# Kernel tuning notes

Measured on AMD Instinct MI355X. Metric: run time of the kernel, lower is better.

The kernel has to match this reference:

```python
import jax, jax.numpy as jnp
import numpy as np

SCALE = 0.08838834764831845  # 1/sqrt(output_dim=128)


def setup_inputs() -> dict:
    key = jax.random.key(0)
    ks = jax.random.split(key, 7)
    N, D, H, E = 4096, 1024, 8, 128
    s = 0.02
    return {
        "X": jax.random.normal(ks[0], (N, D), jnp.float32),
        "Wq": jax.random.normal(ks[1], (H, D, E), jnp.float32) * s,
        "bq": jax.random.normal(ks[2], (H, E), jnp.float32) * s,
        "Wk": jax.random.normal(ks[3], (H, D, E), jnp.float32) * s,
        "bk": jax.random.normal(ks[4], (H, E), jnp.float32) * s,
        "Wv": jax.random.normal(ks[5], (H, D, E), jnp.float32) * s,
        "bv": jax.random.normal(ks[6], (H, E), jnp.float32) * s,
    }


def reference(X, Wq, bq, Wk, bk, Wv, bv):
    # per-head projections, batched over heads: [H, N, E]
    q = jnp.einsum("nd,hde->hne", X, Wq) + bq[:, None, :]
    k = jnp.einsum("nd,hde->hne", X, Wk) + bk[:, None, :]
    v = jnp.einsum("nd,hde->hne", X, Wv) + bv[:, None, :]
    # score[h, n, m] = scale * q[h,n,:] . k[h,m,:]  ([H, N, N])
    score = SCALE * jnp.einsum("hne,hme->hnm", q, k)
    # NOTE: original uses nn.Softmax(dim=0) on the [N, N] per-head matrix,
    # i.e. normalization over the QUERY (row) axis -> axis=1 here.
    attn = jax.nn.softmax(score, axis=1)
    # z[h, n, e] = sum_m attn[h,n,m] * v[h,m,e]
    z = jnp.einsum("hnm,hme->hne", attn, v)
    # concat heads along feature dim: [N, H*E]
    H, N, E = z.shape
    Z = jnp.transpose(z, (1, 0, 2)).reshape(N, H * E)
    return jax.nn.sigmoid(Z)
```

## Files before the change

kernel.cpp:

```cpp
#include <hip/hip_runtime.h>
#include <hip/hip_bf16.h>
#include <stdint.h>

typedef __bf16 bf16_t;
typedef __bf16 bf16x4 __attribute__((ext_vector_type(4)));
typedef __bf16 bf16x8 __attribute__((ext_vector_type(8)));
typedef float f32x4 __attribute__((ext_vector_type(4)));

#define MFMA_16x16x32(A, B, C) __builtin_amdgcn_mfma_f32_16x16x32_bf16(A, B, C, 0, 0, 0)
#define EXP2(x) __builtin_amdgcn_exp2f(x)

static constexpr float kScale = 0.08838834764831845f;
static constexpr float kLog2e = 1.4426950408889634f;
static constexpr float kC1 = kScale * kLog2e;

__device__ __forceinline__ void lds_cp16(void* lds, const void* g) {
  __builtin_amdgcn_global_load_lds(
      (__attribute__((address_space(1))) void*)(uintptr_t)g,
      (__attribute__((address_space(3))) void*)(uintptr_t)lds, 16, 0, 0);
}

template <int R, int K>
__device__ __forceinline__ void stage_tile(bf16_t* lds, const bf16_t* g, int ldg, int tid) {
  constexpr int TOT = R * K;
  constexpr int CH = R * 32;
  constexpr int ITERS = TOT / 2048;
  const int wave = tid >> 6;
#pragma unroll
  for (int i = 0; i < ITERS; ++i) {
    int linear = i * 2048 + tid * 8;
    int chunk = linear / CH;
    int rem = linear % CH;
    int r = rem >> 5;
    int c = rem & 31;
    lds_cp16(lds + i * 2048 + wave * 512, g + r * ldg + chunk * 32 + c);
  }
}

__device__ __forceinline__ bf16x8 frag_ld(const bf16_t* lds_chunk, int row, int lane) {
  return *(const bf16x8*)(lds_chunk + row * 32 + ((lane >> 4) << 3));
}

__device__ __forceinline__ bf16x8 p_transpose(f32x4 pa, f32x4 pb, bool hi16) {
  uint32_t a0, a1, b0, b1;
  asm("v_cvt_pk_bf16_f32 %0, %1, %2" : "=v"(a0) : "v"(pa[0]), "v"(pa[1]));
  asm("v_cvt_pk_bf16_f32 %0, %1, %2" : "=v"(a1) : "v"(pa[2]), "v"(pa[3]));
  asm("v_cvt_pk_bf16_f32 %0, %1, %2" : "=v"(b0) : "v"(pb[0]), "v"(pb[1]));
  asm("v_cvt_pk_bf16_f32 %0, %1, %2" : "=v"(b1) : "v"(pb[2]), "v"(pb[3]));
  asm("v_permlane32_swap_b32 %0, %1" : "+v"(a0), "+v"(b0));
  asm("v_permlane32_swap_b32 %0, %1" : "+v"(a1), "+v"(b1));
  uint32_t sX0 = (uint32_t)__builtin_amdgcn_ds_swizzle((int)a0, 0x401F);
  uint32_t sX1 = (uint32_t)__builtin_amdgcn_ds_swizzle((int)b0, 0x401F);
  uint32_t sY0 = (uint32_t)__builtin_amdgcn_ds_swizzle((int)a1, 0x401F);
  uint32_t sY1 = (uint32_t)__builtin_amdgcn_ds_swizzle((int)b1, 0x401F);
  union {
    uint32_t u[4];
    bf16x8 v;
  } r;
  r.u[0] = hi16 ? sX1 : a0;
  r.u[1] = hi16 ? sY1 : a1;
  r.u[2] = hi16 ? b0 : sX0;
  r.u[3] = hi16 ? b1 : sY0;
  return r.v;
}

__global__ void cvt_kernel(const float* __restrict__ src, bf16_t* __restrict__ dst) {
  const int i = (blockIdx.x * 256 + threadIdx.x) * 4;
  float4 v = *(const float4*)&src[i];
  bf16x4 o;
  o[0] = (bf16_t)v.x;
  o[1] = (bf16_t)v.y;
  o[2] = (bf16_t)v.z;
  o[3] = (bf16_t)v.w;
  *(bf16x4*)&dst[i] = o;
}

__global__ void transpose_qkv_k(const float* __restrict__ Wq, const float* __restrict__ Wk,
                                const float* __restrict__ Wv, bf16_t* __restrict__ Wt) {
  __shared__ alignas(16) bf16_t tile[64][72];
  const int t = threadIdx.x;
  const int z = blockIdx.z;
  const int proj = z >> 3, mat = z & 7;
  const float* src = (proj == 0 ? Wq : proj == 1 ? Wk : Wv);
  const int R = 1024, C = 128;
  const int r0 = blockIdx.x * 64, c0 = blockIdx.y * 64;
  const float* s = src + (size_t)mat * R * C;
  bf16_t* d = Wt + (size_t)proj * 1048576 + (size_t)mat * R * C;
  const int rl = t >> 3, cl = (t & 7) * 8;
#pragma unroll
  for (int half = 0; half < 2; ++half) {
    const int r = r0 + rl + half * 32;
    float4 a = *(const float4*)&s[(size_t)r * C + c0 + cl];
    float4 b = *(const float4*)&s[(size_t)r * C + c0 + cl + 4];
    tile[cl + 0][rl + half * 32] = (bf16_t)a.x;
    tile[cl + 1][rl + half * 32] = (bf16_t)a.y;
    tile[cl + 2][rl + half * 32] = (bf16_t)a.z;
    tile[cl + 3][rl + half * 32] = (bf16_t)a.w;
    tile[cl + 4][rl + half * 32] = (bf16_t)b.x;
    tile[cl + 5][rl + half * 32] = (bf16_t)b.y;
    tile[cl + 6][rl + half * 32] = (bf16_t)b.z;
    tile[cl + 7][rl + half * 32] = (bf16_t)b.w;
  }
  __syncthreads();
  const int cl2 = t >> 3, rl2 = (t & 7) * 8;
  *(bf16x8*)&d[(size_t)(c0 + cl2) * R + r0 + rl2] = *(const bf16x8*)&tile[cl2][rl2];
  *(bf16x8*)&d[(size_t)(c0 + cl2 + 32) * R + r0 + rl2] = *(const bf16x8*)&tile[cl2 + 32][rl2];
}

__global__ __launch_bounds__(256, 2) void proj_kernel(const bf16_t* __restrict__ X,
                                                      const bf16_t* __restrict__ Wt,
                                                      const float* __restrict__ bq,
                                                      const float* __restrict__ bk,
                                                      const float* __restrict__ bv,
                                                      bf16_t* __restrict__ qkv) {
  __shared__ alignas(16) char smem[34816];
  bf16_t* As = (bf16_t*)smem;
  bf16_t* Bs = (bf16_t*)(smem + 16384);
  const int t = threadIdx.x, lane = t & 63, w = t >> 6;
  const int l15 = lane & 15, quad = lane >> 4;
  const int ntile = blockIdx.x, mat = blockIdx.y;
  const bf16_t* a0 = X + (size_t)ntile * 128 * 1024;
  const bf16_t* b0 = Wt + (size_t)mat * 131072;
  f32x4 acc[4][4] = {};
  const int rb = (w >> 1) * 64, cb = (w & 1) * 64;
  for (int k0 = 0; k0 < 1024; k0 += 64) {
    stage_tile<128, 64>(As, a0 + k0, 1024, t);
    stage_tile<128, 64>(Bs, b0 + k0, 1024, t);
    __syncthreads();
#pragma unroll
    for (int kk = 0; kk < 2; ++kk) {
      bf16x8 af[4], bfr[4];
#pragma unroll
      for (int i = 0; i < 4; ++i) af[i] = frag_ld(As + kk * 4096, rb + i * 16 + l15, lane);
#pragma unroll
      for (int j = 0; j < 4; ++j) bfr[j] = frag_ld(Bs + kk * 4096, cb + j * 16 + l15, lane);
#pragma unroll
      for (int i = 0; i < 4; ++i)
#pragma unroll
        for (int j = 0; j < 4; ++j) acc[i][j] = MFMA_16x16x32(af[i], bfr[j], acc[i][j]);
    }
    __syncthreads();
  }
  const int proj = mat >> 3, h = mat & 7;
  const float* bias = (proj == 0 ? bq : proj == 1 ? bk : bv) + h * 128;
  bf16_t* Ct = (bf16_t*)smem;
  bf16_t* dst = qkv + (size_t)proj * 4194304 + (size_t)h * 524288;
  if (proj < 2) {
#pragma unroll
    for (int i = 0; i < 4; ++i)
#pragma unroll
      for (int j = 0; j < 4; ++j) {
        const int e = cb + j * 16 + l15;
        const float bval = bias[e];
#pragma unroll
        for (int r = 0; r < 4; ++r)
          Ct[(rb + i * 16 + quad * 4 + r) * 136 + e] = (bf16_t)(acc[i][j][r] + bval);
      }
    __syncthreads();
#pragma unroll
    for (int u = 0; u < 2; ++u) {
      const int nt = w * 2 + u;
#pragma unroll
      for (int ks = 0; ks < 4; ++ks) {
        bf16x8 f = *(const bf16x8*)&Ct[(nt * 16 + l15) * 136 + ks * 32 + quad * 8];
        *(bf16x8*)&dst[(((size_t)(ntile * 8 + nt)) * 4 + ks) * 512 + lane * 8] = f;
      }
    }
  } else {
#pragma unroll
    for (int i = 0; i < 4; ++i)
#pragma unroll
      for (int j = 0; j < 4; ++j) {
        const int e = cb + j * 16 + l15;
        const float bval = bias[e];
        bf16x4 pv;
#pragma unroll
        for (int r = 0; r < 4; ++r) pv[r] = (bf16_t)(acc[i][j][r] + bval);
        *(bf16x4*)&Ct[e * 136 + rb + i * 16 + quad * 4] = pv;
      }
    __syncthreads();
#pragma unroll
    for (int es = 0; es < 8; ++es) {
      bf16x8 f = *(const bf16x8*)&Ct[(es * 16 + l15) * 136 + w * 32 + quad * 8];
      *(bf16x8*)&dst[(((size_t)(ntile * 4 + w)) * 8 + es) * 512 + lane * 8] = f;
    }
  }
}

__global__ __launch_bounds__(256, 2) void pass_a_kernel(const bf16_t* __restrict__ Qf,
                                                        const bf16_t* __restrict__ Kf,
                                                        float* __restrict__ l2c) {
  __shared__ alignas(16) float csred[4][64];
  const int t = threadIdx.x, lane = t & 63, w = t >> 6;
  const int l15 = lane & 15;
  const int h = blockIdx.x, mtile = blockIdx.y;
  const bf16_t* Qh = Qf + (size_t)h * 524288;
  const bf16_t* Kh = Kf + (size_t)h * 524288;
  bf16x8 kf[16];
#pragma unroll
  for (int mg = 0; mg < 4; ++mg)
#pragma unroll
    for (int ks = 0; ks < 4; ++ks)
      kf[mg * 4 + ks] = *(const bf16x8*)&Kh[((mtile * 4 + mg) * 4 + ks) * 512 + lane * 8];
  float cs[4] = {0.f, 0.f, 0.f, 0.f};
  uint32_t qo = w * 2048 + lane * 8;
  bf16x8 af[4];
#pragma unroll
  for (int ks = 0; ks < 4; ++ks) af[ks] = *(const bf16x8*)&Qh[qo + ks * 512];
  for (int it = 0; it < 64; ++it) {
    f32x4 c[4] = {};
#pragma unroll
    for (int ks = 0; ks < 4; ++ks)
#pragma unroll
      for (int mg = 0; mg < 4; ++mg) c[mg] = MFMA_16x16x32(af[ks], kf[mg * 4 + ks], c[mg]);
    qo += 8192;
#pragma unroll
    for (int ks = 0; ks < 4; ++ks) af[ks] = *(const bf16x8*)&Qh[qo + ks * 512];
#pragma unroll
    for (int mg = 0; mg < 4; ++mg)
#pragma unroll
      for (int r = 0; r < 4; ++r) cs[mg] += EXP2(c[mg][r] * kC1);
  }
#pragma unroll
  for (int mg = 0; mg < 4; ++mg) {
    cs[mg] += __shfl_xor(cs[mg], 16, 64);
    cs[mg] += __shfl_xor(cs[mg], 32, 64);
  }
  if (lane < 16) {
#pragma unroll
    for (int mg = 0; mg < 4; ++mg) csred[w][mg * 16 + lane] = cs[mg];
  }
  __syncthreads();
  if (t < 64)
    l2c[(size_t)h * 4096 + mtile * 64 + t] =
        __builtin_log2f(csred[0][t] + csred[1][t] + csred[2][t] + csred[3][t]);
}

__global__ __launch_bounds__(512, 2) void pass_b_kernel(const bf16_t* __restrict__ Qf,
                                                        const bf16_t* __restrict__ Kf,
                                                        const bf16_t* __restrict__ Vf,
                                                        const float* __restrict__ l2c,
                                                        float* __restrict__ out) {
  __shared__ alignas(16) char smem[131072];
  const int t = threadIdx.x, lane = t & 63, w = t >> 6;
  const int quad = lane >> 4, l15 = lane & 15;
  const bool hi16 = (lane & 16) != 0;
  const int npar = w & 3, mpar = w >> 2;
  const int h = blockIdx.x, ntile = blockIdx.y;
  const bf16_t* Kh = Kf + (size_t)h * 524288;
  const char* VhB = (const char*)(Vf + (size_t)h * 524288);
  const bf16_t* Qh = Qf + (size_t)h * 524288;
  const float* lb = l2c + (size_t)h * 4096;

#pragma unroll
  for (int j = 0; j < 8; ++j) {
    const int off = (w * 8 + j) * 1024;
    lds_cp16(smem + off, VhB + off + lane * 16);
  }
  bf16x8 qf[2][4];
#pragma unroll
  for (int nsub = 0; nsub < 2; ++nsub)
#pragma unroll
    for (int ks = 0; ks < 4; ++ks)
      qf[nsub][ks] =
          *(const bf16x8*)&Qh[((ntile * 8 + npar * 2 + nsub) * 4 + ks) * 512 + lane * 8];
  bf16x8 kf[8];
  {
    const bf16_t* kg = Kh + mpar * 4096;
#pragma unroll
    for (int u = 0; u < 8; ++u) kf[u] = *(const bf16x8*)&kg[u * 512 + lane * 8];
  }
  f32x4 gc0 = *(const f32x4*)&lb[mpar * 32 + quad * 4];
  f32x4 gc1 = *(const f32x4*)&lb[mpar * 32 + 16 + quad * 4];
  f32x4 zacc[2][8] = {};
  __syncthreads();

  f32x4 ccp[2][2] = {};
  __builtin_amdgcn_s_setprio(1);
#pragma unroll
  for (int ks = 0; ks < 4; ++ks)
#pragma unroll
    for (int ms = 0; ms < 2; ++ms)
#pragma unroll
      for (int nsub = 0; nsub < 2; ++nsub)
        ccp[ms][nsub] = MFMA_16x16x32(kf[ms * 4 + ks], qf[nsub][ks], ccp[ms][nsub]);
  __builtin_amdgcn_s_setprio(0);
  {
    const bf16_t* kg = Kh + 8192 + mpar * 4096;
#pragma unroll
    for (int u = 0; u < 8; ++u) kf[u] = *(const bf16x8*)&kg[u * 512 + lane * 8];
  }

  for (int wnd = 0; wnd < 16; ++wnd) {
    const int cur = wnd & 1;
    if (wnd < 15) {
      char* vdst = smem + (cur ^ 1) * 65536;
      const char* vsrc = VhB + (size_t)(wnd + 1) * 65536;
#pragma unroll
      for (int j = 0; j < 8; ++j) {
        const int off = (w * 8 + j) * 1024;
        lds_cp16(vdst + off, vsrc + off + lane * 16);
      }
    }
    __builtin_amdgcn_sched_barrier(0);
#pragma unroll
    for (int sub = 0; sub < 4; ++sub) {
      const int it = wnd * 4 + sub;
      f32x4 ccn[2][2] = {};
      __builtin_amdgcn_s_setprio(1);
#pragma unroll
      for (int ks = 0; ks < 4; ++ks)
#pragma unroll
        for (int ms = 0; ms < 2; ++ms)
#pragma unroll
          for (int nsub = 0; nsub < 2; ++nsub)
            ccn[ms][nsub] = MFMA_16x16x32(kf[ms * 4 + ks], qf[nsub][ks], ccn[ms][nsub]);
      __builtin_amdgcn_s_setprio(0);
      {
        const bf16_t* kg = Kh + (size_t)(it + 2) * 8192 + mpar * 4096;
#pragma unroll
        for (int u = 0; u < 8; ++u) kf[u] = *(const bf16x8*)&kg[u * 512 + lane * 8];
      }
      bf16x8 pf[2];
#pragma unroll
      for (int nsub = 0; nsub < 2; ++nsub) {
        f32x4 pa, pb;
#pragma unroll
        for (int r = 0; r < 4; ++r) pa[r] = EXP2(ccp[0][nsub][r] * kC1 - gc0[r]);
#pragma unroll
        for (int r = 0; r < 4; ++r) pb[r] = EXP2(ccp[1][nsub][r] * kC1 - gc1[r]);
        pf[nsub] = p_transpose(pa, pb, hi16);
      }
      {
        const int stn = (it < 63 ? it + 1 : 63) * 2 + mpar;
        gc0 = *(const f32x4*)&lb[stn * 32 + quad * 4];
        gc1 = *(const f32x4*)&lb[stn * 32 + 16 + quad * 4];
      }
      const bf16_t* vbase = (const bf16_t*)(smem + cur * 65536 + sub * 16384) + mpar * 4096;
      __builtin_amdgcn_s_setprio(1);
#pragma unroll
      for (int es = 0; es < 8; ++es) {
        bf16x8 vf = *(const bf16x8*)&vbase[es * 512 + lane * 8];
#pragma unroll
        for (int nsub = 0; nsub < 2; ++nsub)
          zacc[nsub][es] = MFMA_16x16x32(pf[nsub], vf, zacc[nsub][es]);
      }
      __builtin_amdgcn_s_setprio(0);
#pragma unroll
      for (int ms = 0; ms < 2; ++ms)
#pragma unroll
        for (int nsub = 0; nsub < 2; ++nsub) ccp[ms][nsub] = ccn[ms][nsub];
    }
    asm volatile("s_waitcnt vmcnt(8)" ::: "memory");
    __builtin_amdgcn_s_barrier();
  }
  float* red = (float*)smem;
  if (mpar == 1) {
#pragma unroll
    for (int nsub = 0; nsub < 2; ++nsub)
#pragma unroll
      for (int es = 0; es < 8; ++es)
        *(f32x4*)&red[npar * 4096 + (nsub * 8 + es) * 256 + lane * 4] = zacc[nsub][es];
  }
  __syncthreads();
  if (mpar == 0) {
#pragma unroll
    for (int nsub = 0; nsub < 2; ++nsub) {
#pragma unroll
      for (int es = 0; es < 8; ++es) {
        f32x4 o = *(const f32x4*)&red[npar * 4096 + (nsub * 8 + es) * 256 + lane * 4];
        const int e = es * 16 + l15;
#pragma unroll
        for (int r = 0; r < 4; ++r) {
          const int n = ntile * 128 + npar * 32 + nsub * 16 + quad * 4 + r;
          const float z = zacc[nsub][es][r] + o[r];
          out[(size_t)n * 1024 + h * 128 + e] = 1.f / (1.f + EXP2(-z * kLog2e));
        }
      }
    }
  }
}

extern "C" void kernel_launch(void* const* d_in, const int* in_sizes, int n_in, void* d_out,
                              int out_size, void* d_ws, size_t ws_size, hipStream_t stream) {
  (void)in_sizes;
  (void)n_in;
  (void)out_size;
  (void)ws_size;
  const float* X = (const float*)d_in[0];
  const float* Wq = (const float*)d_in[1];
  const float* bq = (const float*)d_in[2];
  const float* Wk = (const float*)d_in[3];
  const float* bk = (const float*)d_in[4];
  const float* Wv = (const float*)d_in[5];
  const float* bv = (const float*)d_in[6];
  float* out = (float*)d_out;
  char* ws = (char*)d_ws;
  bf16_t* Qf = (bf16_t*)(ws);
  bf16_t* Kf = (bf16_t*)(ws + 8388608);
  bf16_t* Vf = (bf16_t*)(ws + 16777216);
  bf16_t* Xb = (bf16_t*)(ws + 25165824);
  bf16_t* Wt = (bf16_t*)(ws + 33554432);
  float* l2c = (float*)(ws + 39845888);

  cvt_kernel<<<4096, 256, 0, stream>>>(X, Xb);
  transpose_qkv_k<<<dim3(16, 2, 24), 256, 0, stream>>>(Wq, Wk, Wv, Wt);
  proj_kernel<<<dim3(32, 24), 256, 0, stream>>>(Xb, Wt, bq, bk, bv, Qf);
  pass_a_kernel<<<dim3(8, 64), 256, 0, stream>>>(Qf, Kf, l2c);
  pass_b_kernel<<<dim3(8, 32), 512, 0, stream>>>(Qf, Kf, Vf, l2c, out);
}
```

Baseline: 234.4 us.

## Load V fragments directly from global into registers instead of LDS double-buffering

```diff
diff --git a/kernel.cpp b/kernel.cpp
--- a/kernel.cpp
+++ b/kernel.cpp
@@ -241,22 +241,17 @@
                                                         const bf16_t* __restrict__ Vf,
                                                         const float* __restrict__ l2c,
                                                         float* __restrict__ out) {
-  __shared__ alignas(16) char smem[131072];
+  __shared__ alignas(16) char smem[65536];
   const int t = threadIdx.x, lane = t & 63, w = t >> 6;
   const int quad = lane >> 4, l15 = lane & 15;
   const bool hi16 = (lane & 16) != 0;
   const int npar = w & 3, mpar = w >> 2;
   const int h = blockIdx.x, ntile = blockIdx.y;
   const bf16_t* Kh = Kf + (size_t)h * 524288;
-  const char* VhB = (const char*)(Vf + (size_t)h * 524288);
+  const bf16_t* Vh = Vf + (size_t)h * 524288;
   const bf16_t* Qh = Qf + (size_t)h * 524288;
   const float* lb = l2c + (size_t)h * 4096;
 
-#pragma unroll
-  for (int j = 0; j < 8; ++j) {
-    const int off = (w * 8 + j) * 1024;
-    lds_cp16(smem + off, VhB + off + lane * 16);
-  }
   bf16x8 qf[2][4];
 #pragma unroll
   for (int nsub = 0; nsub < 2; ++nsub)
@@ -273,7 +268,6 @@
   f32x4 gc0 = *(const f32x4*)&lb[mpar * 32 + quad * 4];
   f32x4 gc1 = *(const f32x4*)&lb[mpar * 32 + 16 + quad * 4];
   f32x4 zacc[2][8] = {};
-  __syncthreads();
 
   f32x4 ccp[2][2] = {};
   __builtin_amdgcn_s_setprio(1);
@@ -291,68 +285,55 @@
     for (int u = 0; u < 8; ++u) kf[u] = *(const bf16x8*)&kg[u * 512 + lane * 8];
   }
 
-  for (int wnd = 0; wnd < 16; ++wnd) {
-    const int cur = wnd & 1;
-    if (wnd < 15) {
-      char* vdst = smem + (cur ^ 1) * 65536;
-      const char* vsrc = VhB + (size_t)(wnd + 1) * 65536;
-#pragma unroll
-      for (int j = 0; j < 8; ++j) {
-        const int off = (w * 8 + j) * 1024;
-        lds_cp16(vdst + off, vsrc + off + lane * 16);
-      }
-    }
-    __builtin_amdgcn_sched_barrier(0);
-#pragma unroll
-    for (int sub = 0; sub < 4; ++sub) {
-      const int it = wnd * 4 + sub;
-      f32x4 ccn[2][2] = {};
-      __builtin_amdgcn_s_setprio(1);
-#pragma unroll
-      for (int ks = 0; ks < 4; ++ks)
-#pragma unroll
-        for (int ms = 0; ms < 2; ++ms)
-#pragma unroll
-          for (int nsub = 0; nsub < 2; ++nsub)
-            ccn[ms][nsub] = MFMA_16x16x32(kf[ms * 4 + ks], qf[nsub][ks], ccn[ms][nsub]);
-      __builtin_amdgcn_s_setprio(0);
-      {
-        const bf16_t* kg = Kh + (size_t)(it + 2) * 8192 + mpar * 4096;
-#pragma unroll
-        for (int u = 0; u < 8; ++u) kf[u] = *(const bf16x8*)&kg[u * 512 + lane * 8];
-      }
-      bf16x8 pf[2];
-#pragma unroll
-      for (int nsub = 0; nsub < 2; ++nsub) {
-        f32x4 pa, pb;
-#pragma unroll
-        for (int r = 0; r < 4; ++r) pa[r] = EXP2(ccp[0][nsub][r] * kC1 - gc0[r]);
-#pragma unroll
-        for (int r = 0; r < 4; ++r) pb[r] = EXP2(ccp[1][nsub][r] * kC1 - gc1[r]);
-        pf[nsub] = p_transpose(pa, pb, hi16);
-      }
-      {
-        const int stn = (it < 63 ? it + 1 : 63) * 2 + mpar;
-        gc0 = *(const f32x4*)&lb[stn * 32 + quad * 4];
-        gc1 = *(const f32x4*)&lb[stn * 32 + 16 + quad * 4];
-      }
-      const bf16_t* vbase = (const bf16_t*)(smem + cur * 65536 + sub * 16384) + mpar * 4096;
-      __builtin_amdgcn_s_setprio(1);
-#pragma unroll
-      for (int es = 0; es < 8; ++es) {
-        bf16x8 vf = *(const bf16x8*)&vbase[es * 512 + lane * 8];
+  for (int it = 0; it < 64; ++it) {
+    bf16x8 vfr[8];
+    {
+      const bf16_t* vg = Vh + (size_t)it * 8192 + mpar * 4096;
+#pragma unroll
+      for (int es = 0; es < 8; ++es) vfr[es] = *(const bf16x8*)&vg[es * 512 + lane * 8];
+    }
+    f32x4 ccn[2][2] = {};
+    __builtin_amdgcn_s_setprio(1);
+#pragma unroll
+    for (int ks = 0; ks < 4; ++ks)
+#pragma unroll
+      for (int ms = 0; ms < 2; ++ms)
 #pragma unroll
         for (int nsub = 0; nsub < 2; ++nsub)
-          zacc[nsub][es] = MFMA_16x16x32(pf[nsub], vf, zacc[nsub][es]);
-      }
-      __builtin_amdgcn_s_setprio(0);
-#pragma unroll
-      for (int ms = 0; ms < 2; ++ms)
-#pragma unroll
-        for (int nsub = 0; nsub < 2; ++nsub) ccp[ms][nsub] = ccn[ms][nsub];
-    }
-    asm volatile("s_waitcnt vmcnt(8)" ::: "memory");
-    __builtin_amdgcn_s_barrier();
+          ccn[ms][nsub] = MFMA_16x16x32(kf[ms * 4 + ks], qf[nsub][ks], ccn[ms][nsub]);
+    __builtin_amdgcn_s_setprio(0);
+    {
+      const bf16_t* kg = Kh + (size_t)(it + 2) * 8192 + mpar * 4096;
+#pragma unroll
+      for (int u = 0; u < 8; ++u) kf[u] = *(const bf16x8*)&kg[u * 512 + lane * 8];
+    }
+    bf16x8 pf[2];
+#pragma unroll
+    for (int nsub = 0; nsub < 2; ++nsub) {
+      f32x4 pa, pb;
+#pragma unroll
+      for (int r = 0; r < 4; ++r) pa[r] = EXP2(ccp[0][nsub][r] * kC1 - gc0[r]);
+#pragma unroll
+      for (int r = 0; r < 4; ++r) pb[r] = EXP2(ccp[1][nsub][r] * kC1 - gc1[r]);
+      pf[nsub] = p_transpose(pa, pb, hi16);
+    }
+    {
+      const int stn = (it < 63 ? it + 1 : 63) * 2 + mpar;
+      gc0 = *(const f32x4*)&lb[stn * 32 + quad * 4];
+      gc1 = *(const f32x4*)&lb[stn * 32 + 16 + quad * 4];
+    }
+    __builtin_amdgcn_s_setprio(1);
+#pragma unroll
+    for (int es = 0; es < 8; ++es) {
+#pragma unroll
+      for (int nsub = 0; nsub < 2; ++nsub)
+        zacc[nsub][es] = MFMA_16x16x32(pf[nsub], vfr[es], zacc[nsub][es]);
+    }
+    __builtin_amdgcn_s_setprio(0);
+#pragma unroll
+    for (int ms = 0; ms < 2; ++ms)
+#pragma unroll
+      for (int nsub = 0; nsub < 2; ++nsub) ccp[ms][nsub] = ccn[ms][nsub];
   }
   float* red = (float*)smem;
   if (mpar == 1) {
```

Measured after the change: 235.3 us, median of 2. Within noise of the previous version (+0.4%).
